# Kernel optimization log

Hardware: AMD Instinct MI355X
Metric: run time of the kernel (lower is better)

The kernel has to match this reference:

```python
import jax, jax.numpy as jnp
import numpy as np

FFT_LEN = 256
BATCH = 65536


def _dft_kernels():
    n = np.arange(FFT_LEN)
    k = n.reshape(-1, 1)
    cos_k = np.cos(2 * np.pi * k * n / FFT_LEN).astype(np.float32)   # [K, N]
    sin_k = (-np.sin(2 * np.pi * k * n / FFT_LEN)).astype(np.float32)  # [K, N], note the minus sign
    return jnp.asarray(cos_k), jnp.asarray(sin_k)


def setup_inputs() -> dict:
    key = jax.random.key(0)
    x = jax.random.normal(key, (BATCH, 2, FFT_LEN), dtype=jnp.float32)
    cos_kernel, sin_kernel = _dft_kernels()
    return {"x": x, "cos_kernel": cos_kernel, "sin_kernel": sin_kernel}


def reference(x, cos_kernel, sin_kernel):
    # x: [B, 2, 256] -> real/imag channels. Conv1d(kernel=256, no pad) over L=256
    # is exactly a dense 256x256 matmul per channel (a direct O(n^2) DFT).
    x_real = x[:, 0, :]  # [B, 256]
    x_imag = x[:, 1, :]  # [B, 256]
    # real_conv(v) = cos_kernel @ v ; imag_conv(v) = sin_kernel @ v
    real_part = jnp.einsum('kn,bn->bk', cos_kernel, x_real) - jnp.einsum('kn,bn->bk', sin_kernel, x_imag)
    imag_part = jnp.einsum('kn,bn->bk', cos_kernel, x_imag) + jnp.einsum('kn,bn->bk', sin_kernel, x_real)
    out = jnp.concatenate([real_part, imag_part], axis=1)  # [B, 512]
    return out[:, :, None]  # [B, 512, 1] matches torch conv output length 1
```

## Files before the change

kernel.cpp:

```cpp
#include <hip/hip_runtime.h>
#include <hip/hip_bf16.h>
#include <stdint.h>


typedef __attribute__((ext_vector_type(8))) short bf16x8;
typedef __attribute__((ext_vector_type(4))) float f32x4;

#define KDIM 512
#define NDIM 512
#define BM 64

__device__ __forceinline__ ushort f2bf(float f) {
  union { float f; uint32_t u; } v; v.f = f;
  uint32_t r = (v.u + 0x7fffu + ((v.u >> 16) & 1u)) >> 16;
  return (ushort)r;
}

__global__ __launch_bounds__(512) void build_w_kernel(const float* __restrict__ cosk,
                                                      const float* __restrict__ sink,
                                                      ushort* __restrict__ Wf) {
  int g = blockIdx.x * 512 + threadIdx.x;
  int lane = g & 63;
  int nt = (g >> 6) & 31;
  int j = nt * 16 + (lane & 15);
  int kbase = (g >> 11) * 32 + (lane >> 4) * 8;
  bf16x8 w8;
#pragma unroll
  for (int e = 0; e < 8; ++e) {
    int k = kbase + e;
    float v;
    if (j < 256) {
      v = (k < 256) ? cosk[(j << 8) + k] : -sink[(j << 8) + (k - 256)];
    } else {
      int jj = j - 256;
      v = (k < 256) ? sink[(jj << 8) + k] : cosk[(jj << 8) + (k - 256)];
    }
    w8[e] = (short)f2bf(v);
  }
  *reinterpret_cast<bf16x8*>(Wf + (size_t)g * 8) = w8;
}

__device__ __forceinline__ bf16x8 cvt8(f32x4 a, f32x4 b) {
  bf16x8 w8;
  w8[0] = (short)f2bf(a[0]); w8[1] = (short)f2bf(a[1]);
  w8[2] = (short)f2bf(a[2]); w8[3] = (short)f2bf(a[3]);
  w8[4] = (short)f2bf(b[0]); w8[5] = (short)f2bf(b[1]);
  w8[6] = (short)f2bf(b[2]); w8[7] = (short)f2bf(b[3]);
  return w8;
}

__global__ __launch_bounds__(512) void dft_gemm_kernel(const float* __restrict__ A,
                                                       const ushort* __restrict__ Wf,
                                                       float* __restrict__ out) {
  __shared__ ushort As[2][BM * 64];

  const int tid  = threadIdx.x;
  const int lane = tid & 63;
  const int wid  = tid >> 6;
  const int m0   = blockIdx.x * BM;
  const int c0   = wid * 64;

  const int srow = tid >> 3;
  const int skq  = (tid & 7) * 8;
  const float* ap = A + (size_t)(m0 + srow) * KDIM + skq;
  const int swidx = (srow << 6) + (skq ^ ((srow & 7) << 3));

  const int lrow = lane & 15;
  const int lk8  = (lane >> 4) * 8;

  const ushort* wp = Wf + (size_t)(c0 >> 4) * 512 + lane * 8;

  f32x4 acc[4][4] = {};

  f32x4 q0 = *reinterpret_cast<const f32x4*>(ap);
  f32x4 q1 = *reinterpret_cast<const f32x4*>(ap + 4);
  f32x4 p0 = *reinterpret_cast<const f32x4*>(ap + 64);
  f32x4 p1 = *reinterpret_cast<const f32x4*>(ap + 68);
  *reinterpret_cast<bf16x8*>(&As[0][swidx]) = cvt8(q0, q1);
  asm volatile("s_waitcnt lgkmcnt(0)" ::: "memory");
  __builtin_amdgcn_s_barrier();

#pragma unroll
  for (int t = 0; t < 8; ++t) {
    if (t < 7)
      *reinterpret_cast<bf16x8*>(&As[(t + 1) & 1][swidx]) = cvt8(p0, p1);

    bf16x8 wfr[2][4];
#pragma unroll
    for (int kk = 0; kk < 2; ++kk)
#pragma unroll
      for (int mi = 0; mi < 4; ++mi)
        wfr[kk][mi] = *reinterpret_cast<const bf16x8*>(
            wp + (size_t)((t * 2 + kk) * 32 + mi) * 512);

    if (t < 6) {
      p0 = *reinterpret_cast<const f32x4*>(ap + (t + 2) * 64);
      p1 = *reinterpret_cast<const f32x4*>(ap + (t + 2) * 64 + 4);
    }

#pragma unroll
    for (int kk = 0; kk < 2; ++kk) {
      bf16x8 xfr[4];
#pragma unroll
      for (int ni = 0; ni < 4; ++ni) {
        int row = ni * 16 + lrow;
        int idx = (row << 6) + ((kk * 32 + lk8) ^ ((lrow & 7) << 3));
        xfr[ni] = *reinterpret_cast<const bf16x8*>(&As[t & 1][idx]);
      }
#pragma unroll
      for (int mi = 0; mi < 4; ++mi)
#pragma unroll
        for (int ni = 0; ni < 4; ++ni)
          acc[mi][ni] = __builtin_amdgcn_mfma_f32_16x16x32_bf16(
              wfr[kk][mi], xfr[ni], acc[mi][ni], 0, 0, 0);
    }

    if (t < 7) {
      asm volatile("s_waitcnt lgkmcnt(0)" ::: "memory");
      __builtin_amdgcn_s_barrier();
    }
  }

  const int jbase = c0 + (lane >> 4) * 4;
#pragma unroll
  for (int ni = 0; ni < 4; ++ni) {
    size_t rowb = (size_t)(m0 + ni * 16 + lrow) * NDIM;
#pragma unroll
    for (int mi = 0; mi < 4; ++mi)
      *reinterpret_cast<f32x4*>(out + rowb + jbase + mi * 16) = acc[mi][ni];
  }
}

extern "C" void kernel_launch(void* const* d_in, const int* in_sizes, int n_in,
                              void* d_out, int out_size, void* d_ws, size_t ws_size,
                              hipStream_t stream) {
  const float* x    = (const float*)d_in[0];
  const float* cosk = (const float*)d_in[1];
  const float* sink = (const float*)d_in[2];
  float* out = (float*)d_out;
  ushort* Wf = (ushort*)d_ws;

  build_w_kernel<<<64, 512, 0, stream>>>(cosk, sink, Wf);
  dft_gemm_kernel<<<65536 / BM, 512, 0, stream>>>(x, Wf, out);
}
```

Baseline: 72.74 us.

## Tile GEMM by 512 rows × 64 output columns with W slice staged in LDS

```diff
diff --git a/kernel.cpp b/kernel.cpp
--- a/kernel.cpp
+++ b/kernel.cpp
@@ -8,7 +8,6 @@
 
 #define KDIM 512
 #define NDIM 512
-#define BM 64
 
 __device__ __forceinline__ ushort f2bf(float f) {
   union { float f; uint32_t u; } v; v.f = f;
@@ -49,82 +48,103 @@
   return w8;
 }
 
+__device__ __forceinline__ void gload_lds16(const ushort* g, ushort* l) {
+  __builtin_amdgcn_global_load_lds(
+      (__attribute__((address_space(1))) const void*)g,
+      (__attribute__((address_space(3))) void*)l, 16, 0, 0);
+}
+
 __global__ __launch_bounds__(512) void dft_gemm_kernel(const float* __restrict__ A,
                                                        const ushort* __restrict__ Wf,
                                                        float* __restrict__ out) {
-  __shared__ ushort As[2][BM * 64];
+  __shared__ ushort Ws[16 * 256 * 8];
+  __shared__ ushort Xs[512 * 64];
 
   const int tid  = threadIdx.x;
   const int lane = tid & 63;
   const int wid  = tid >> 6;
-  const int m0   = blockIdx.x * BM;
-  const int c0   = wid * 64;
-
-  const int srow = tid >> 3;
-  const int skq  = (tid & 7) * 8;
-  const float* ap = A + (size_t)(m0 + srow) * KDIM + skq;
-  const int swidx = (srow << 6) + (skq ^ ((srow & 7) << 3));
-
+  const int p    = blockIdx.x;
+  const int xcd  = p & 7;
+  const int r    = p >> 3;
+  const int q    = r & 7;
+  const int s    = (r >> 3) * 8 + xcd;
+  const int m0   = s * 512;
   const int lrow = lane & 15;
   const int lk8  = (lane >> 4) * 8;
 
-  const ushort* wp = Wf + (size_t)(c0 >> 4) * 512 + lane * 8;
+#pragma unroll
+  for (int rr = 0; rr < 8; ++rr) {
+    int cb  = rr * 512 + wid * 64;
+    int c   = cb + lane;
+    int k5  = c >> 8;
+    int off = c & 255;
+    gload_lds16(Wf + ((size_t)k5 * 2048 + q * 256 + off) * 8,
+                Ws + (size_t)cb * 8);
+  }
+
+  const float* ap = A + (size_t)(m0 + tid) * KDIM;
+  f32x4 xr[16];
+#pragma unroll
+  for (int i = 0; i < 16; ++i)
+    xr[i] = *reinterpret_cast<const f32x4*>(ap + i * 4);
+
+#pragma unroll
+  for (int s8 = 0; s8 < 8; ++s8) {
+    int idx = (tid << 6) + ((s8 ^ (tid & 7)) << 3);
+    *reinterpret_cast<bf16x8*>(&Xs[idx]) = cvt8(xr[2 * s8], xr[2 * s8 + 1]);
+  }
+  asm volatile("s_waitcnt vmcnt(0) lgkmcnt(0)" ::: "memory");
+  __builtin_amdgcn_s_barrier();
 
   f32x4 acc[4][4] = {};
 
-  f32x4 q0 = *reinterpret_cast<const f32x4*>(ap);
-  f32x4 q1 = *reinterpret_cast<const f32x4*>(ap + 4);
-  f32x4 p0 = *reinterpret_cast<const f32x4*>(ap + 64);
-  f32x4 p1 = *reinterpret_cast<const f32x4*>(ap + 68);
-  *reinterpret_cast<bf16x8*>(&As[0][swidx]) = cvt8(q0, q1);
-  asm volatile("s_waitcnt lgkmcnt(0)" ::: "memory");
-  __builtin_amdgcn_s_barrier();
-
 #pragma unroll
   for (int t = 0; t < 8; ++t) {
-    if (t < 7)
-      *reinterpret_cast<bf16x8*>(&As[(t + 1) & 1][swidx]) = cvt8(p0, p1);
-
-    bf16x8 wfr[2][4];
+    if (t < 7) {
+      const float* apn = ap + (t + 1) * 64;
 #pragma unroll
-    for (int kk = 0; kk < 2; ++kk)
-#pragma unroll
-      for (int mi = 0; mi < 4; ++mi)
-        wfr[kk][mi] = *reinterpret_cast<const bf16x8*>(
-            wp + (size_t)((t * 2 + kk) * 32 + mi) * 512);
-
-    if (t < 6) {
-      p0 = *reinterpret_cast<const f32x4*>(ap + (t + 2) * 64);
-      p1 = *reinterpret_cast<const f32x4*>(ap + (t + 2) * 64 + 4);
+      for (int i = 0; i < 16; ++i)
+        xr[i] = *reinterpret_cast<const f32x4*>(apn + i * 4);
     }
 
 #pragma unroll
     for (int kk = 0; kk < 2; ++kk) {
-      bf16x8 xfr[4];
+      bf16x8 wfr[4], xfr[4];
+#pragma unroll
+      for (int mi = 0; mi < 4; ++mi)
+        wfr[mi] = *reinterpret_cast<const bf16x8*>(
+            &Ws[(size_t)(((t * 2 + kk) * 256) + mi * 64 + lane) * 8]);
 #pragma unroll
       for (int ni = 0; ni < 4; ++ni) {
-        int row = ni * 16 + lrow;
-        int idx = (row << 6) + ((kk * 32 + lk8) ^ ((lrow & 7) << 3));
-        xfr[ni] = *reinterpret_cast<const bf16x8*>(&As[t & 1][idx]);
+        int row = wid * 64 + ni * 16 + lrow;
+        int idx = (row << 6) + ((kk * 32 + lk8) ^ ((row & 7) << 3));
+        xfr[ni] = *reinterpret_cast<const bf16x8*>(&Xs[idx]);
       }
 #pragma unroll
       for (int mi = 0; mi < 4; ++mi)
 #pragma unroll
         for (int ni = 0; ni < 4; ++ni)
           acc[mi][ni] = __builtin_amdgcn_mfma_f32_16x16x32_bf16(
-              wfr[kk][mi], xfr[ni], acc[mi][ni], 0, 0, 0);
+              wfr[mi], xfr[ni], acc[mi][ni], 0, 0, 0);
     }
 
     if (t < 7) {
       asm volatile("s_waitcnt lgkmcnt(0)" ::: "memory");
       __builtin_amdgcn_s_barrier();
+#pragma unroll
+      for (int s8 = 0; s8 < 8; ++s8) {
+        int idx = (tid << 6) + ((s8 ^ (tid & 7)) << 3);
+        *reinterpret_cast<bf16x8*>(&Xs[idx]) = cvt8(xr[2 * s8], xr[2 * s8 + 1]);
+      }
+      asm volatile("s_waitcnt lgkmcnt(0)" ::: "memory");
+      __builtin_amdgcn_s_barrier();
     }
   }
 
-  const int jbase = c0 + (lane >> 4) * 4;
+  const int jbase = q * 64 + (lane >> 4) * 4;
 #pragma unroll
   for (int ni = 0; ni < 4; ++ni) {
-    size_t rowb = (size_t)(m0 + ni * 16 + lrow) * NDIM;
+    size_t rowb = (size_t)(m0 + wid * 64 + ni * 16 + lrow) * NDIM;
 #pragma unroll
     for (int mi = 0; mi < 4; ++mi)
       *reinterpret_cast<f32x4*>(out + rowb + jbase + mi * 16) = acc[mi][ni];
@@ -141,5 +161,5 @@
   ushort* Wf = (ushort*)d_ws;
 
   build_w_kernel<<<64, 512, 0, stream>>>(cosk, sink, Wf);
-  dft_gemm_kernel<<<65536 / BM, 512, 0, stream>>>(x, Wf, out);
+  dft_gemm_kernel<<<1024, 512, 0, stream>>>(x, Wf, out);
 }
```

Measured after the change: 183.7 us. +152.6%, slower.
